# Performance work log

Hardware: AMD Instinct MI355X
Metric: run time of the kernel (lower is better)

## Reference

```python
import jax, jax.numpy as jnp
import numpy as np

B, N, DIM, H, DH = 4, 2048, 1024, 16, 64  # batch, seq, model dim, heads, head dim


def setup_inputs() -> dict:
    key = jax.random.key(0)
    k1, k2, k3 = jax.random.split(key, 3)
    x = jax.random.normal(k1, (B, N, DIM), dtype=jnp.float32)
    w_qkv = jax.random.normal(k2, (DIM, 3 * H * DH), dtype=jnp.float32) * (DIM ** -0.5)
    w_out = jax.random.normal(k3, (H * DH, DIM), dtype=jnp.float32) * ((H * DH) ** -0.5)
    b_out = jnp.zeros((DIM,), dtype=jnp.float32)
    return {"x": x, "w_qkv": w_qkv, "w_out": w_out, "b_out": b_out}


def reference(x, w_qkv, w_out, b_out):
    scale = DH ** -0.5
    qkv = x @ w_qkv                              # [b, n, 3*h*d]
    q, k, v = jnp.split(qkv, 3, axis=-1)
    # 'b n (h d) -> b h n d'
    def to_heads(t):
        return t.reshape(B, N, H, DH).transpose(0, 2, 1, 3)
    q, k, v = to_heads(q), to_heads(k), to_heads(v)
    dots = jnp.einsum('bhid,bhjd->bhij', q, k) * scale   # [b, h, n, n]
    attn = jax.nn.softmax(dots, axis=-1)
    out = jnp.einsum('bhij,bhjd->bhid', attn, v)          # [b, h, n, d]
    out = out.transpose(0, 2, 1, 3).reshape(B, N, H * DH) # 'b h n d -> b n (h d)'
    return out @ w_out + b_out
```

## Files before the change

kernel.cpp:

```cpp
#include <hip/hip_runtime.h>
#include <stdint.h>

#define B_    4
#define N_    2048
#define DIM_  1024
#define H_    16
#define DH_   64
#define BN_   (B_ * N_)
#define QKVN_ (3 * H_ * DH_)

#define AS1_ __attribute__((address_space(1)))
#define AS3_ __attribute__((address_space(3)))

typedef unsigned short u16;
typedef __attribute__((ext_vector_type(8)))  __bf16 bf16x8;
typedef __attribute__((ext_vector_type(8)))  short  short8;
typedef __attribute__((ext_vector_type(4)))  float  f32x4;
typedef __attribute__((ext_vector_type(16))) float  f32x16;
typedef __attribute__((ext_vector_type(4)))  u16    u16x4;

__device__ inline u16 f2bf(float f) {
    union { __bf16 b; u16 u; } v; v.b = (__bf16)f; return v.u;
}
__device__ inline float bf2f(u16 u) {
    union { uint32_t u; float f; } v; v.u = ((uint32_t)u) << 16;
    return v.f;
}

__global__ __launch_bounds__(256) void cast_f32_bf16(const float* __restrict__ in,
                                                     u16* __restrict__ out, int n4) {
    int i = blockIdx.x * blockDim.x + threadIdx.x;
    int stride = gridDim.x * blockDim.x;
    for (; i < n4; i += stride) {
        float4 v = reinterpret_cast<const float4*>(in)[i];
        u16x4 o;
        o.x = f2bf(v.x); o.y = f2bf(v.y); o.z = f2bf(v.z); o.w = f2bf(v.w);
        reinterpret_cast<u16x4*>(out)[i] = o;
    }
}

__global__ __launch_bounds__(256) void transpose_cast(const float* __restrict__ in,
                                                      u16* __restrict__ out, int R, int C) {
    int gid = blockIdx.x * blockDim.x + threadIdx.x;
    int total = C * (R / 4);
    if (gid >= total) return;
    int n  = gid % C;
    int k4 = (gid / C) * 4;
    u16x4 o;
    o.x = f2bf(in[(size_t)(k4 + 0) * C + n]);
    o.y = f2bf(in[(size_t)(k4 + 1) * C + n]);
    o.z = f2bf(in[(size_t)(k4 + 2) * C + n]);
    o.w = f2bf(in[(size_t)(k4 + 3) * C + n]);
    *reinterpret_cast<u16x4*>(&out[(size_t)n * R + k4]) = o;
}

template <bool BF16_OUT>
__global__ __launch_bounds__(256) void gemm_bt(const u16* __restrict__ A,
                                               const u16* __restrict__ BT,
                                               void* __restrict__ Cout,
                                               const float* __restrict__ bias,
                                               int M, int Nn, int K) {
    __shared__ __align__(16) u16 AsF[128 * 32];
    __shared__ __align__(16) u16 BsF[128 * 32];

    const int tid  = threadIdx.x;
    const int m0   = blockIdx.y * 128;
    const int n0   = blockIdx.x * 128;
    const int w    = tid >> 6;
    const int lane = tid & 63;
    const int lr   = lane & 15;
    const int lg   = lane >> 4;
    const int wm   = w >> 1;
    const int wn   = w & 1;

    f32x4 acc[4][4] = {};

    const int sr = tid >> 2;
    const int sc = (tid & 3) * 8;
    const u16* Aptr = A  + (size_t)(m0 + sr) * K + sc;
    const u16* Bptr = BT + (size_t)(n0 + sr) * K + sc;
    const int ldsb = w * 512;

    for (int kt = 0; kt < K; kt += 32) {
        __builtin_amdgcn_global_load_lds((const AS1_ void*)(Aptr + kt),
                                         (AS3_ void*)&AsF[ldsb], 16, 0, 0);
        __builtin_amdgcn_global_load_lds((const AS1_ void*)(Aptr + (size_t)64 * K + kt),
                                         (AS3_ void*)&AsF[2048 + ldsb], 16, 0, 0);
        __builtin_amdgcn_global_load_lds((const AS1_ void*)(Bptr + kt),
                                         (AS3_ void*)&BsF[ldsb], 16, 0, 0);
        __builtin_amdgcn_global_load_lds((const AS1_ void*)(Bptr + (size_t)64 * K + kt),
                                         (AS3_ void*)&BsF[2048 + ldsb], 16, 0, 0);
        __syncthreads();

        bf16x8 af[4], bfr[4];
#pragma unroll
        for (int m = 0; m < 4; m++)
            af[m] = *reinterpret_cast<const bf16x8*>(&AsF[(wm * 64 + m * 16 + lr) * 32 + lg * 8]);
#pragma unroll
        for (int n = 0; n < 4; n++)
            bfr[n] = *reinterpret_cast<const bf16x8*>(&BsF[(wn * 64 + n * 16 + lr) * 32 + lg * 8]);
#pragma unroll
        for (int m = 0; m < 4; m++)
#pragma unroll
            for (int n = 0; n < 4; n++)
                acc[m][n] = __builtin_amdgcn_mfma_f32_16x16x32_bf16(af[m], bfr[n], acc[m][n], 0, 0, 0);
        __syncthreads();
    }

#pragma unroll
    for (int m = 0; m < 4; m++)
#pragma unroll
        for (int n = 0; n < 4; n++) {
            const int row = m0 + wm * 64 + m * 16 + lg * 4;
            const int col = n0 + wn * 64 + n * 16 + lr;
#pragma unroll
            for (int r = 0; r < 4; r++) {
                if (BF16_OUT) {
                    ((u16*)Cout)[(size_t)(row + r) * Nn + col] = f2bf(acc[m][n][r]);
                } else {
                    ((float*)Cout)[(size_t)(row + r) * Nn + col] = acc[m][n][r] + bias[col];
                }
            }
        }
}

__global__ __launch_bounds__(256) void attn_kernel(const u16* __restrict__ qkv,
                                                   u16* __restrict__ out) {
    __shared__ __align__(16) u16      KsS[64 * 64];
    __shared__ __align__(16) uint32_t VTs[64 * 32];
    __shared__ __align__(16) uint32_t PsW[4 * 32 * 36];

    const int tid  = threadIdx.x;
    const int w    = tid >> 6;
    const int lane = tid & 63;
    const int q32  = lane & 31;
    const int hi   = lane >> 5;

    const int bh = blockIdx.y;
    const int b  = bh >> 4;
    const int h  = bh & 15;
    const int rowbase = b * N_;
    const int qglob = blockIdx.x * 128 + w * 32 + q32;
    const int qoff  = h * DH_;
    const float qs = 0.125f * 1.4426950408889634f;

    bf16x8 qf[4];
    {
        const u16* qp = qkv + (size_t)(rowbase + qglob) * QKVN_ + qoff;
#pragma unroll
        for (int ks = 0; ks < 4; ks++)
            qf[ks] = *reinterpret_cast<const bf16x8*>(qp + ks * 16 + hi * 8);
    }

    int kch[4], vrd[4];
#pragma unroll
    for (int ks = 0; ks < 4; ks++) {
        kch[ks] = ((2 * ks + hi) ^ (q32 & 7)) * 8;
        vrd[ks] = (ks * 8 + hi * 4) ^ ((q32 & 7) << 2);
    }
    const int krowA = q32 * 64;
    const int krowB = (32 + q32) * 64;
    const int vrowA = q32 * 32;
    const int vrowB = (32 + q32) * 32;
    const int psw   = w * 1152 + q32 * 36;
    const int pswW  = psw + 2 * hi;
    const int pswR  = psw + 4 * hi;

    float mrun = -3e38f, lrun = 0.f;
    f32x16 o0, o1;
#pragma unroll
    for (int r = 0; r < 16; r++) { o0[r] = 0.f; o1[r] = 0.f; }

    const u16* kg = qkv + (size_t)rowbase * QKVN_ + DIM_ + qoff;
    const u16* vg = qkv + (size_t)rowbase * QKVN_ + 2 * DIM_ + qoff;

    const int kr = tid >> 2, ka = tid & 3;
    const size_t kgo = (size_t)kr * QKVN_ + ka * 16;
    const int kl0 = kr * 64 + ((2 * ka)     ^ (kr & 7)) * 8;
    const int kl1 = kr * 64 + ((2 * ka + 1) ^ (kr & 7)) * 8;
    const int vp = tid >> 3, vd = (tid & 7) * 8;
    const size_t vgo0 = (size_t)(2 * vp) * QKVN_ + vd;
    const size_t vgo1 = vgo0 + QKVN_;

    short8 kst0, kst1, vst0, vst1;
    kst0 = *reinterpret_cast<const short8*>(kg + kgo);
    kst1 = *reinterpret_cast<const short8*>(kg + kgo + 8);
    vst0 = *reinterpret_cast<const short8*>(vg + vgo0);
    vst1 = *reinterpret_cast<const short8*>(vg + vgo1);

    *reinterpret_cast<short8*>(&KsS[kl0]) = kst0;
    *reinterpret_cast<short8*>(&KsS[kl1]) = kst1;
    {
        const u16* v0 = reinterpret_cast<const u16*>(&vst0);
        const u16* v1 = reinterpret_cast<const u16*>(&vst1);
#pragma unroll
        for (int i = 0; i < 8; i++)
            VTs[(vd + i) * 32 + (vp ^ (i << 2))] = (uint32_t)v0[i] | ((uint32_t)v1[i] << 16);
    }
    __syncthreads();

    for (int t = 0; t < N_ / 64; t++) {
        if (t + 1 < N_ / 64) {
            const u16* kg2 = kg + (size_t)(t + 1) * 64 * QKVN_;
            const u16* vg2 = vg + (size_t)(t + 1) * 64 * QKVN_;
            kst0 = *reinterpret_cast<const short8*>(kg2 + kgo);
            kst1 = *reinterpret_cast<const short8*>(kg2 + kgo + 8);
            vst0 = *reinterpret_cast<const short8*>(vg2 + vgo0);
            vst1 = *reinterpret_cast<const short8*>(vg2 + vgo1);
        }

        f32x16 sa0, sa1;
#pragma unroll
        for (int r = 0; r < 16; r++) { sa0[r] = 0.f; sa1[r] = 0.f; }
#pragma unroll
        for (int ks = 0; ks < 4; ks++) {
            bf16x8 a0 = *reinterpret_cast<const bf16x8*>(&KsS[krowA + kch[ks]]);
            bf16x8 a1 = *reinterpret_cast<const bf16x8*>(&KsS[krowB + kch[ks]]);
            sa0 = __builtin_amdgcn_mfma_f32_32x32x16_bf16(a0, qf[ks], sa0, 0, 0, 0);
            sa1 = __builtin_amdgcn_mfma_f32_32x32x16_bf16(a1, qf[ks], sa1, 0, 0, 0);
        }

        float tmax = sa0[0];
#pragma unroll
        for (int r = 1; r < 16; r++) tmax = fmaxf(tmax, sa0[r]);
#pragma unroll
        for (int r = 0; r < 16; r++) tmax = fmaxf(tmax, sa1[r]);
        tmax = fmaxf(tmax, __shfl_xor(tmax, 32));
        const float ts = tmax * qs;

        if (!__all(ts - mrun <= 8.f)) {
            float mnew = fmaxf(mrun, ts);
            float fac  = exp2f(mrun - mnew);
            mrun = mnew;
            lrun *= fac;
#pragma unroll
            for (int r = 0; r < 16; r++) { o0[r] *= fac; o1[r] *= fac; }
        }

        float psum = 0.f;
#pragma unroll
        for (int r = 0; r < 16; r++) {
            sa0[r] = exp2f(__builtin_fmaf(sa0[r], qs, -mrun));
            psum += sa0[r];
        }
#pragma unroll
        for (int r = 0; r < 16; r++) {
            sa1[r] = exp2f(__builtin_fmaf(sa1[r], qs, -mrun));
            psum += sa1[r];
        }
        psum += __shfl_xor(psum, 32);
        lrun += psum;

#pragma unroll
        for (int j = 0; j < 4; j++) {
            u16x4 pw;
            pw.x = f2bf(sa0[4 * j + 0]); pw.y = f2bf(sa0[4 * j + 1]);
            pw.z = f2bf(sa0[4 * j + 2]); pw.w = f2bf(sa0[4 * j + 3]);
            *reinterpret_cast<u16x4*>(&PsW[pswW + 4 * j]) = pw;
        }
#pragma unroll
        for (int j = 0; j < 4; j++) {
            u16x4 pw;
            pw.x = f2bf(sa1[4 * j + 0]); pw.y = f2bf(sa1[4 * j + 1]);
            pw.z = f2bf(sa1[4 * j + 2]); pw.w = f2bf(sa1[4 * j + 3]);
            *reinterpret_cast<u16x4*>(&PsW[pswW + 16 + 4 * j]) = pw;
        }

#pragma unroll
        for (int ks = 0; ks < 4; ks++) {
            bf16x8 pb  = *reinterpret_cast<const bf16x8*>(&PsW[pswR + ks * 8]);
            bf16x8 va0 = *reinterpret_cast<const bf16x8*>(&VTs[vrowA + vrd[ks]]);
            bf16x8 va1 = *reinterpret_cast<const bf16x8*>(&VTs[vrowB + vrd[ks]]);
            o0 = __builtin_amdgcn_mfma_f32_32x32x16_bf16(va0, pb, o0, 0, 0, 0);
            o1 = __builtin_amdgcn_mfma_f32_32x32x16_bf16(va1, pb, o1, 0, 0, 0);
        }

        __syncthreads();
        if (t + 1 < N_ / 64) {
            *reinterpret_cast<short8*>(&KsS[kl0]) = kst0;
            *reinterpret_cast<short8*>(&KsS[kl1]) = kst1;
            const u16* v0 = reinterpret_cast<const u16*>(&vst0);
            const u16* v1 = reinterpret_cast<const u16*>(&vst1);
#pragma unroll
            for (int i = 0; i < 8; i++)
                VTs[(vd + i) * 32 + (vp ^ (i << 2))] = (uint32_t)v0[i] | ((uint32_t)v1[i] << 16);
        }
        __syncthreads();
    }

    const float linv = 1.f / lrun;
    u16* orow = out + (size_t)(rowbase + qglob) * DIM_ + qoff;
#pragma unroll
    for (int j = 0; j < 4; j++) {
        u16x4 ov;
        ov.x = f2bf(o0[4 * j + 0] * linv); ov.y = f2bf(o0[4 * j + 1] * linv);
        ov.z = f2bf(o0[4 * j + 2] * linv); ov.w = f2bf(o0[4 * j + 3] * linv);
        *reinterpret_cast<u16x4*>(&orow[8 * j + 4 * hi]) = ov;
        u16x4 ow;
        ow.x = f2bf(o1[4 * j + 0] * linv); ow.y = f2bf(o1[4 * j + 1] * linv);
        ow.z = f2bf(o1[4 * j + 2] * linv); ow.w = f2bf(o1[4 * j + 3] * linv);
        *reinterpret_cast<u16x4*>(&orow[32 + 8 * j + 4 * hi]) = ow;
    }
}

extern "C" void kernel_launch(void* const* d_in, const int* in_sizes, int n_in,
                              void* d_out, int out_size, void* d_ws, size_t ws_size,
                              hipStream_t stream) {
    const float* x     = (const float*)d_in[0];
    const float* w_qkv = (const float*)d_in[1];
    const float* w_out = (const float*)d_in[2];
    const float* b_out = (const float*)d_in[3];
    float* out = (float*)d_out;

    char* ws = (char*)d_ws;
    u16* xbf   = (u16*)(ws);
    u16* wqkvT = (u16*)(ws + 16777216);
    u16* woutT = (u16*)(ws + 23068672);
    u16* qkv   = (u16*)(ws + 25165824);
    u16* attnO = (u16*)(ws + 75497472);

    cast_f32_bf16<<<2048, 256, 0, stream>>>(x, xbf, (BN_ * DIM_) / 4);
    transpose_cast<<<(DIM_ / 4) * QKVN_ / 256, 256, 0, stream>>>(w_qkv, wqkvT, DIM_, QKVN_);
    transpose_cast<<<(DIM_ / 4) * DIM_ / 256, 256, 0, stream>>>(w_out, woutT, DIM_, DIM_);

    gemm_bt<true><<<dim3(QKVN_ / 128, BN_ / 128), 256, 0, stream>>>(
        xbf, wqkvT, qkv, nullptr, BN_, QKVN_, DIM_);

    attn_kernel<<<dim3(N_ / 128, B_ * H_), 256, 0, stream>>>(qkv, attnO);

    gemm_bt<false><<<dim3(DIM_ / 128, BN_ / 128), 256, 0, stream>>>(
        attnO, woutT, out, b_out, BN_, DIM_, DIM_);
}
```

Baseline: 346.7 us.

## Add XCD-aware block swizzle, MFMA priority hints, V-tile LDS swizzle, tree max

Both GEMMs and the attention kernel now launch a 1D grid and remap block ids so consecutive tiles land on the same XCD, to improve L2 reuse of shared weight and K/V data. s_setprio is raised around the MFMA loops so waves issuing matrix work are favoured over waves doing loads or softmax. The V transpose layout in LDS gets a new rotation-based XOR swizzle meant to cut bank conflicts on writes and reads. The row-max reduction becomes a shallower tree to shorten the dependency chain. These are several unrelated tweaks, and the swizzle remap assumes grid sizes divisible by 8.

```diff
diff --git a/kernel.cpp b/kernel.cpp
--- a/kernel.cpp
+++ b/kernel.cpp
@@ -25,6 +25,9 @@
 __device__ inline float bf2f(u16 u) {
     union { uint32_t u; float f; } v; v.u = ((uint32_t)u) << 16;
     return v.f;
+}
+__device__ inline int xcd_swz(int bid, int nwg) {
+    return (bid & 7) * (nwg >> 3) + (bid >> 3);
 }
 
 __global__ __launch_bounds__(256) void cast_f32_bf16(const float* __restrict__ in,
@@ -63,9 +66,13 @@
     __shared__ __align__(16) u16 AsF[128 * 32];
     __shared__ __align__(16) u16 BsF[128 * 32];
 
+    const int nbx = Nn >> 7;
+    int bid = blockIdx.x;
+    if ((gridDim.x & 7) == 0) bid = xcd_swz(bid, gridDim.x);
+    const int m0 = (bid / nbx) * 128;
+    const int n0 = (bid % nbx) * 128;
+
     const int tid  = threadIdx.x;
-    const int m0   = blockIdx.y * 128;
-    const int n0   = blockIdx.x * 128;
     const int w    = tid >> 6;
     const int lane = tid & 63;
     const int lr   = lane & 15;
@@ -99,11 +106,13 @@
 #pragma unroll
         for (int n = 0; n < 4; n++)
             bfr[n] = *reinterpret_cast<const bf16x8*>(&BsF[(wn * 64 + n * 16 + lr) * 32 + lg * 8]);
+        __builtin_amdgcn_s_setprio(1);
 #pragma unroll
         for (int m = 0; m < 4; m++)
 #pragma unroll
             for (int n = 0; n < 4; n++)
                 acc[m][n] = __builtin_amdgcn_mfma_f32_16x16x32_bf16(af[m], bfr[n], acc[m][n], 0, 0, 0);
+        __builtin_amdgcn_s_setprio(0);
         __syncthreads();
     }
 
@@ -136,11 +145,12 @@
     const int q32  = lane & 31;
     const int hi   = lane >> 5;
 
-    const int bh = blockIdx.y;
+    int bid = xcd_swz(blockIdx.x, gridDim.x);
+    const int bh = bid >> 4;
     const int b  = bh >> 4;
     const int h  = bh & 15;
     const int rowbase = b * N_;
-    const int qglob = blockIdx.x * 128 + w * 32 + q32;
+    const int qglob = (bid & 15) * 128 + w * 32 + q32;
     const int qoff  = h * DH_;
     const float qs = 0.125f * 1.4426950408889634f;
 
@@ -152,16 +162,17 @@
             qf[ks] = *reinterpret_cast<const bf16x8*>(qp + ks * 16 + hi * 8);
     }
 
-    int kch[4], vrd[4];
+    int kch[4], vrd0[4], vrd1[4];
+    const int f0 = (((q32 >> 3) + q32) & 7) << 2;
+    const int f1 = (((q32 >> 3) + q32 + 4) & 7) << 2;
 #pragma unroll
     for (int ks = 0; ks < 4; ks++) {
-        kch[ks] = ((2 * ks + hi) ^ (q32 & 7)) * 8;
-        vrd[ks] = (ks * 8 + hi * 4) ^ ((q32 & 7) << 2);
+        kch[ks]  = ((2 * ks + hi) ^ (q32 & 7)) * 8;
+        vrd0[ks] = q32 * 32        + ((ks * 8 + hi * 4) ^ f0);
+        vrd1[ks] = (32 + q32) * 32 + ((ks * 8 + hi * 4) ^ f1);
     }
     const int krowA = q32 * 64;
     const int krowB = (32 + q32) * 64;
-    const int vrowA = q32 * 32;
-    const int vrowB = (32 + q32) * 32;
     const int psw   = w * 1152 + q32 * 36;
     const int pswW  = psw + 2 * hi;
     const int pswR  = psw + 4 * hi;
@@ -178,8 +189,8 @@
     const size_t kgo = (size_t)kr * QKVN_ + ka * 16;
     const int kl0 = kr * 64 + ((2 * ka)     ^ (kr & 7)) * 8;
     const int kl1 = kr * 64 + ((2 * ka + 1) ^ (kr & 7)) * 8;
-    const int vp = tid >> 3, vd = (tid & 7) * 8;
-    const size_t vgo0 = (size_t)(2 * vp) * QKVN_ + vd;
+    const int vp = tid >> 3, vk = tid & 7;
+    const size_t vgo0 = (size_t)(2 * vp) * QKVN_ + vk * 8;
     const size_t vgo1 = vgo0 + QKVN_;
 
     short8 kst0, kst1, vst0, vst1;
@@ -195,7 +206,8 @@
         const u16* v1 = reinterpret_cast<const u16*>(&vst1);
 #pragma unroll
         for (int i = 0; i < 8; i++)
-            VTs[(vd + i) * 32 + (vp ^ (i << 2))] = (uint32_t)v0[i] | ((uint32_t)v1[i] << 16);
+            VTs[(vk * 8 + i) * 32 + (vp ^ (((vk + i) & 7) << 2))] =
+                (uint32_t)v0[i] | ((uint32_t)v1[i] << 16);
     }
     __syncthreads();
 
@@ -212,6 +224,7 @@
         f32x16 sa0, sa1;
 #pragma unroll
         for (int r = 0; r < 16; r++) { sa0[r] = 0.f; sa1[r] = 0.f; }
+        __builtin_amdgcn_s_setprio(1);
 #pragma unroll
         for (int ks = 0; ks < 4; ks++) {
             bf16x8 a0 = *reinterpret_cast<const bf16x8*>(&KsS[krowA + kch[ks]]);
@@ -219,12 +232,24 @@
             sa0 = __builtin_amdgcn_mfma_f32_32x32x16_bf16(a0, qf[ks], sa0, 0, 0, 0);
             sa1 = __builtin_amdgcn_mfma_f32_32x32x16_bf16(a1, qf[ks], sa1, 0, 0, 0);
         }
-
-        float tmax = sa0[0];
-#pragma unroll
-        for (int r = 1; r < 16; r++) tmax = fmaxf(tmax, sa0[r]);
-#pragma unroll
-        for (int r = 0; r < 16; r++) tmax = fmaxf(tmax, sa1[r]);
+        __builtin_amdgcn_s_setprio(0);
+
+        float m0a = fmaxf(fmaxf(sa0[0], sa0[1]), sa0[2]);
+        float m1a = fmaxf(fmaxf(sa0[3], sa0[4]), sa0[5]);
+        float m2a = fmaxf(fmaxf(sa0[6], sa0[7]), sa0[8]);
+        float m3a = fmaxf(fmaxf(sa0[9], sa0[10]), sa0[11]);
+        float m4a = fmaxf(fmaxf(sa0[12], sa0[13]), sa0[14]);
+        float m5a = fmaxf(fmaxf(sa0[15], sa1[0]), sa1[1]);
+        float m6a = fmaxf(fmaxf(sa1[2], sa1[3]), sa1[4]);
+        float m7a = fmaxf(fmaxf(sa1[5], sa1[6]), sa1[7]);
+        float m8a = fmaxf(fmaxf(sa1[8], sa1[9]), sa1[10]);
+        float m9a = fmaxf(fmaxf(sa1[11], sa1[12]), sa1[13]);
+        float mAa = fmaxf(sa1[14], sa1[15]);
+        float t0 = fmaxf(fmaxf(m0a, m1a), m2a);
+        float t1 = fmaxf(fmaxf(m3a, m4a), m5a);
+        float t2 = fmaxf(fmaxf(m6a, m7a), m8a);
+        float t3 = fmaxf(m9a, mAa);
+        float tmax = fmaxf(fmaxf(t0, t1), fmaxf(t2, t3));
         tmax = fmaxf(tmax, __shfl_xor(tmax, 32));
         const float ts = tmax * qs;
 
@@ -266,14 +291,16 @@
             *reinterpret_cast<u16x4*>(&PsW[pswW + 16 + 4 * j]) = pw;
         }
 
+        __builtin_amdgcn_s_setprio(1);
 #pragma unroll
         for (int ks = 0; ks < 4; ks++) {
             bf16x8 pb  = *reinterpret_cast<const bf16x8*>(&PsW[pswR + ks * 8]);
-            bf16x8 va0 = *reinterpret_cast<const bf16x8*>(&VTs[vrowA + vrd[ks]]);
-            bf16x8 va1 = *reinterpret_cast<const bf16x8*>(&VTs[vrowB + vrd[ks]]);
+            bf16x8 va0 = *reinterpret_cast<const bf16x8*>(&VTs[vrd0[ks]]);
+            bf16x8 va1 = *reinterpret_cast<const bf16x8*>(&VTs[vrd1[ks]]);
             o0 = __builtin_amdgcn_mfma_f32_32x32x16_bf16(va0, pb, o0, 0, 0, 0);
             o1 = __builtin_amdgcn_mfma_f32_32x32x16_bf16(va1, pb, o1, 0, 0, 0);
         }
+        __builtin_amdgcn_s_setprio(0);
 
         __syncthreads();
         if (t + 1 < N_ / 64) {
@@ -283,7 +310,8 @@
             const u16* v1 = reinterpret_cast<const u16*>(&vst1);
 #pragma unroll
             for (int i = 0; i < 8; i++)
-                VTs[(vd + i) * 32 + (vp ^ (i << 2))] = (uint32_t)v0[i] | ((uint32_t)v1[i] << 16);
+                VTs[(vk * 8 + i) * 32 + (vp ^ (((vk + i) & 7) << 2))] =
+                    (uint32_t)v0[i] | ((uint32_t)v1[i] << 16);
         }
         __syncthreads();
     }
@@ -323,11 +351,11 @@
     transpose_cast<<<(DIM_ / 4) * QKVN_ / 256, 256, 0, stream>>>(w_qkv, wqkvT, DIM_, QKVN_);
     transpose_cast<<<(DIM_ / 4) * DIM_ / 256, 256, 0, stream>>>(w_out, woutT, DIM_, DIM_);
 
-    gemm_bt<true><<<dim3(QKVN_ / 128, BN_ / 128), 256, 0, stream>>>(
+    gemm_bt<true><<<(QKVN_ / 128) * (BN_ / 128), 256, 0, stream>>>(
         xbf, wqkvT, qkv, nullptr, BN_, QKVN_, DIM_);
 
-    attn_kernel<<<dim3(N_ / 128, B_ * H_), 256, 0, stream>>>(qkv, attnO);
-
-    gemm_bt<false><<<dim3(DIM_ / 128, BN_ / 128), 256, 0, stream>>>(
+    attn_kernel<<<(N_ / 128) * (B_ * H_), 256, 0, stream>>>(qkv, attnO);
+
+    gemm_bt<false><<<(DIM_ / 128) * (BN_ / 128), 256, 0, stream>>>(
         attnO, woutT, out, b_out, BN_, DIM_, DIM_);
 }
```

Measured after the change: 317.2 us. -8.5%, faster.
